# Optimization experiments

Measured on AMD Instinct MI355X. Metric: run time of the kernel, lower is better.

The kernel has to match this reference:

```python
import jax, jax.numpy as jnp
import numpy as np

N = 20000
E = 100000
EB = 20000
WIDTH = 32
KER_W = 64
KER_IN = 6
DEPTH = 4


def setup_inputs() -> dict:
    key = jax.random.key(0)
    ks = jax.random.split(key, 24)
    d = {}
    d["x"] = jax.random.normal(ks[0], (N, 1), dtype=jnp.float32)
    d["edge_index"] = jax.random.randint(ks[1], (2, E), 0, N)
    d["edge_attr"] = jax.random.uniform(ks[2], (E, KER_IN), dtype=jnp.float32)
    d["edge_index_boundary"] = jax.random.randint(ks[3], (2, EB), 0, N)
    d["edge_attr_boundary"] = jax.random.uniform(ks[4], (EB, KER_IN), dtype=jnp.float32)
    s = 0.1
    d["fc1_w"] = jax.random.normal(ks[5], (1, WIDTH), dtype=jnp.float32) * s
    d["fc1_b"] = jnp.zeros((WIDTH,), jnp.float32)
    d["fc2_w"] = jax.random.normal(ks[6], (WIDTH, 1), dtype=jnp.float32) * s
    d["fc2_b"] = jnp.zeros((1,), jnp.float32)
    for i, pfx in enumerate(["k1", "k2"]):
        o = 7 + i * 5
        d[pfx + "_w1"] = jax.random.normal(ks[o], (KER_IN, KER_W), dtype=jnp.float32) * s
        d[pfx + "_b1"] = jnp.zeros((KER_W,), jnp.float32)
        d[pfx + "_w2"] = jax.random.normal(ks[o + 1], (KER_W, KER_W), dtype=jnp.float32) * s
        d[pfx + "_b2"] = jnp.zeros((KER_W,), jnp.float32)
        d[pfx + "_w3"] = jax.random.normal(ks[o + 2], (KER_W, WIDTH * WIDTH), dtype=jnp.float32) * s
        d[pfx + "_b3"] = jnp.zeros((WIDTH * WIDTH,), jnp.float32)
        d[("root1", "root2")[i]] = jax.random.normal(ks[o + 3], (WIDTH, WIDTH), dtype=jnp.float32) * s
        d[("bias1", "bias2")[i]] = jnp.zeros((WIDTH,), jnp.float32)
    return d


def _nnconv(h, ei, ea, w1, b1, w2, b2, w3, b3, root, bias):
    # kernel MLP on edge_attr -> per-edge [in, out] weight
    k = jax.nn.relu(ea @ w1 + b1)
    k = jax.nn.relu(k @ w2 + b2)
    w = (k @ w3 + b3).reshape(-1, WIDTH, WIDTH)  # [E, in, out]
    msg = jnp.einsum('ei,eio->eo', h[ei[0]], w)  # gather + per-edge matmul
    agg = jax.ops.segment_sum(msg, ei[1], num_segments=N)
    cnt = jax.ops.segment_sum(jnp.ones((ei.shape[1],), h.dtype), ei[1], num_segments=N)
    agg = agg / jnp.maximum(cnt, 1.0)[:, None]  # mean aggregation
    return agg + h @ root + bias


def reference(x, edge_index, edge_attr, edge_index_boundary, edge_attr_boundary,
              fc1_w, fc1_b, fc2_w, fc2_b,
              k1_w1, k1_b1, k1_w2, k1_b2, k1_w3, k1_b3, root1, bias1,
              k2_w1, k2_b1, k2_w2, k2_b2, k2_w3, k2_b3, root2, bias2):
    h0 = x @ fc1_w + fc1_b  # fc1(data.x), reused every depth step
    h = h0
    for _ in range(DEPTH):
        h = (_nnconv(h, edge_index, edge_attr, k1_w1, k1_b1, k1_w2, k1_b2, k1_w3, k1_b3, root1, bias1)
             + _nnconv(h, edge_index_boundary, edge_attr_boundary, k2_w1, k2_b1, k2_w2, k2_b2, k2_w3, k2_b3, root2, bias2))
        h = jax.nn.relu(h) + h0
    return h @ fc2_w + fc2_b
```

## Files before the change

kernel.cpp:

```cpp
#include <hip/hip_runtime.h>
#include <cstdint>
#include <cstddef>

#define NN    20000
#define EM    100000
#define EBN   20000
#define WID   32
#define KW    64
#define KIN   6
#define NDEPTH 4
#define GC    2080
#define NBL   6
#define GR    2084
#define NQ    520
#define TPB_F 576


__global__ void k_count4(const int* __restrict__ ei, const int* __restrict__ eib,
                         int* __restrict__ cs1, int* __restrict__ cnt1,
                         int* __restrict__ csb, int* __restrict__ cntb) {
    int t = blockIdx.x * blockDim.x + threadIdx.x;
    if (t < EM) atomicAdd(&cs1[ei[t]], 1);
    else if (t < 2 * EM) atomicAdd(&cnt1[ei[t]], 1);
    else if (t < 2 * EM + EBN) atomicAdd(&csb[eib[t - 2 * EM]], 1);
    else if (t < 2 * EM + 2 * EBN) atomicAdd(&cntb[eib[t - 2 * EM]], 1);
}

__global__ void k_inv2(const int* __restrict__ cnt1, float* __restrict__ inv1,
                       const int* __restrict__ cntb, float* __restrict__ invb) {
    int i = blockIdx.x * blockDim.x + threadIdx.x;
    if (i < NN) {
        int c = cnt1[i]; if (c < 1) c = 1;
        inv1[i] = 1.0f / (float)c;
    } else if (i < 2 * NN) {
        int c = cntb[i - NN]; if (c < 1) c = 1;
        invb[i - NN] = 1.0f / (float)c;
    }
}


__global__ __launch_bounds__(1024) void k_scan3(
        const int* __restrict__ csA, int* __restrict__ curA, int* __restrict__ arankA,
        int* __restrict__ anodesA, int* __restrict__ aoffA, int* __restrict__ dnaA, int EA,
        const int* __restrict__ csB, int* __restrict__ curB, int* __restrict__ arankB,
        int* __restrict__ anodesB, int* __restrict__ aoffB, int* __restrict__ dnaB, int EB) {
    __shared__ int part[1024];
    __shared__ int partf[1024];
    const int* cnt; int *cur, *arank, *anodes, *aoff, *dna; int E;
    if (blockIdx.x == 0) { cnt = csA; cur = curA; arank = arankA; anodes = anodesA; aoff = aoffA; dna = dnaA; E = EA; }
    else                 { cnt = csB; cur = curB; arank = arankB; anodes = anodesB; aoff = aoffB; dna = dnaB; E = EB; }
    int t = threadIdx.x;
    int per = (NN + 1023) / 1024;
    int base = t * per;
    int s = 0, f = 0;
    for (int i = 0; i < per; i++) {
        int idx = base + i;
        if (idx < NN) { int c = cnt[idx]; s += c; f += (c > 0) ? 1 : 0; }
    }
    part[t] = s; partf[t] = f;
    __syncthreads();
    for (int od = 1; od < 1024; od <<= 1) {
        int v  = (t >= od) ? part[t - od] : 0;
        int vf = (t >= od) ? partf[t - od] : 0;
        __syncthreads();
        part[t] += v; partf[t] += vf;
        __syncthreads();
    }
    int run  = (t > 0) ? part[t - 1] : 0;
    int runf = (t > 0) ? partf[t - 1] : 0;
    for (int i = 0; i < per; i++) {
        int idx = base + i;
        if (idx < NN) {
            int c = cnt[idx];
            cur[idx] = run;
            arank[idx] = runf;
            if (c > 0) { anodes[runf] = idx; aoff[runf] = run; runf++; }
            run += c;
        }
    }
    if (t == 1023) { dna[0] = partf[1023]; aoff[partf[1023]] = E; }
}


__global__ void k_scatter3(const int* __restrict__ ei, int* __restrict__ cur1,
                           int* __restrict__ perm1, const int* __restrict__ eib,
                           int* __restrict__ curb, int* __restrict__ permb) {
    int t = blockIdx.x * blockDim.x + threadIdx.x;
    if (t < EM) { int p = atomicAdd(&cur1[ei[t]], 1); perm1[p] = t; }
    else if (t < EM + EBN) {
        int e = t - EM;
        int p = atomicAdd(&curb[eib[e]], 1); permb[p] = e;
    }
}

__global__ void k_permidx3(const int* __restrict__ ei, const int* __restrict__ perm1,
                           const int* __restrict__ arank1, int* __restrict__ rk1,
                           int* __restrict__ dst1,
                           const int* __restrict__ eib, const int* __restrict__ permb,
                           const int* __restrict__ arankb, int* __restrict__ rkb,
                           int* __restrict__ dstb) {
    int t = blockIdx.x * blockDim.x + threadIdx.x;
    if (t < EM) {
        int e = perm1[t];
        rk1[t] = arank1[ei[e]];
        dst1[t] = ei[EM + e];
    } else if (t < EM + EBN) {
        int i = t - EM;
        int e = permb[i];
        rkb[i] = arankb[eib[e]];
        dstb[i] = eib[EBN + e];
    }
}


__global__ void k_permM3(const float* __restrict__ w3a, const float* __restrict__ b3a,
                         float* __restrict__ M1,
                         const float* __restrict__ w3b, const float* __restrict__ b3b,
                         float* __restrict__ M2,
                         const float* __restrict__ r1, const float* __restrict__ b1,
                         const float* __restrict__ r2, const float* __restrict__ b2,
                         float* __restrict__ rs, float* __restrict__ bs) {
    int t = blockIdx.x * blockDim.x + threadIdx.x;
    if (t < 32 * GC) {
        int i = t / GC, c = t % GC;
        M1[t] = (c < 2048) ? w3a[(c >> 5) * 1024 + i * 32 + (c & 31)]
                           : b3a[i * 32 + (c - 2048)];
    } else if (t < 64 * GC) {
        int u = t - 32 * GC;
        int i = u / GC, c = u % GC;
        M2[u] = (c < 2048) ? w3b[(c >> 5) * 1024 + i * 32 + (c & 31)]
                           : b3b[i * 32 + (c - 2048)];
    } else if (t < 64 * GC + 1024) {
        int i = t - 64 * GC;
        rs[i] = r1[i] + r2[i];
    } else if (t < 64 * GC + 1056) {
        int i = t - 64 * GC - 1024;
        bs[i] = b1[i] + b2[i];
    }
}


__global__ __launch_bounds__(256) void k_mlp3(
        const float* __restrict__ ea1, const int* __restrict__ perm1,
        const float* __restrict__ w1a, const float* __restrict__ b1a,
        const float* __restrict__ w2a, const float* __restrict__ b2a,
        float* __restrict__ K1,
        const float* __restrict__ ea2, const int* __restrict__ permb,
        const float* __restrict__ w1b, const float* __restrict__ b1b,
        const float* __restrict__ w2b, const float* __restrict__ b2b,
        float* __restrict__ K2, int nmb) {
    __shared__ float sw1[KIN * KW];
    __shared__ float sw2[KW * KW];
    __shared__ float sb1[KW];
    __shared__ float sb2[KW];
    const float *ea, *w1, *b1, *w2, *b2;
    const int* perm;
    float* K;
    int e, E;
    if ((int)blockIdx.x < nmb) {
        ea = ea1; perm = perm1; w1 = w1a; b1 = b1a; w2 = w2a; b2 = b2a; K = K1;
        e = blockIdx.x * 256 + threadIdx.x; E = EM;
    } else {
        ea = ea2; perm = permb; w1 = w1b; b1 = b1b; w2 = w2b; b2 = b2b; K = K2;
        e = (blockIdx.x - nmb) * 256 + threadIdx.x; E = EBN;
    }
    for (int i = threadIdx.x; i < KIN * KW; i += 256) sw1[i] = w1[i];
    for (int i = threadIdx.x; i < KW * KW; i += 256)  sw2[i] = w2[i];
    if (threadIdx.x < KW) { sb1[threadIdx.x] = b1[threadIdx.x]; sb2[threadIdx.x] = b2[threadIdx.x]; }
    __syncthreads();
    if (e >= E) return;
    int eo = perm[e];
    float a0 = ea[(size_t)eo * KIN + 0];
    float a1 = ea[(size_t)eo * KIN + 1];
    float a2 = ea[(size_t)eo * KIN + 2];
    float a3 = ea[(size_t)eo * KIN + 3];
    float a4 = ea[(size_t)eo * KIN + 4];
    float a5 = ea[(size_t)eo * KIN + 5];
    float t[KW];
#pragma unroll
    for (int j = 0; j < KW; j++) {
        float s = sb1[j];
        s += a0 * sw1[0 * KW + j];
        s += a1 * sw1[1 * KW + j];
        s += a2 * sw1[2 * KW + j];
        s += a3 * sw1[3 * KW + j];
        s += a4 * sw1[4 * KW + j];
        s += a5 * sw1[5 * KW + j];
        t[j] = fmaxf(s, 0.0f);
    }
#pragma unroll
    for (int h = 0; h < 2; h++) {
        int j0 = h * 32;
        float4 acc[8];
#pragma unroll
        for (int jj = 0; jj < 8; jj++)
            acc[jj] = *(const float4*)&sb2[j0 + jj * 4];
#pragma unroll
        for (int c = 0; c < KW; c++) {
            float tc = t[c];
#pragma unroll
            for (int jj = 0; jj < 8; jj++) {
                float4 w = *(const float4*)&sw2[c * KW + j0 + jj * 4];
                acc[jj].x += tc * w.x; acc[jj].y += tc * w.y;
                acc[jj].z += tc * w.z; acc[jj].w += tc * w.w;
            }
        }
#pragma unroll
        for (int jj = 0; jj < 8; jj++) {
            float4 r = acc[jj];
            r.x = fmaxf(r.x, 0.f); r.y = fmaxf(r.y, 0.f);
            r.z = fmaxf(r.z, 0.f); r.w = fmaxf(r.w, 0.f);
            *(float4*)&K[(size_t)e * KW + j0 + jj * 4] = r;
        }
    }
}


__global__ void k_h0g(const float* __restrict__ x, const float* __restrict__ fc1w,
        const float* __restrict__ fc1b, float* __restrict__ h,
        const int* __restrict__ arank1, const int* __restrict__ anodes1,
        const int* __restrict__ dna1, float* __restrict__ hg1,
        const int* __restrict__ arankb, const int* __restrict__ anodesb,
        const int* __restrict__ dnab, float* __restrict__ hgb) {
    int t = blockIdx.x * blockDim.x + threadIdx.x;
    if (t < NN * WID) {
        int n = t >> 5, j = t & 31;
        float v = x[n] * fc1w[j] + fc1b[j];
        h[t] = v;
        int r = arank1[n];
        if (r < dna1[0] && anodes1[r] == n)
            hg1[(r / NBL) * 256 + j * 8 + (r % NBL)] = v;
    } else if (t < 2 * NN * WID) {
        int u = t - NN * WID;
        int n = u >> 5, j = u & 31;
        int r = arankb[n];
        if (r < dnab[0] && anodesb[r] == n)
            hgb[(r / NBL) * 256 + j * 8 + (r % NBL)] = x[n] * fc1w[j] + fc1b[j];
    }
}


__global__ __launch_bounds__(TPB_F, 3) void k_fuse3(
        const int* __restrict__ rkA, const int* __restrict__ dstA,
        const int* __restrict__ aoffA, const int* __restrict__ dnaA,
        const float* __restrict__ KA, const float* __restrict__ MA,
        const float* __restrict__ hgA, float* __restrict__ aggA,
        const int* __restrict__ rkB, const int* __restrict__ dstB,
        const int* __restrict__ aoffB, const int* __restrict__ dnaB,
        const float* __restrict__ KB, const float* __restrict__ MB,
        const float* __restrict__ hgB, float* __restrict__ aggB,
        int nblkA) {
    __shared__ float sG[NBL * GR];
    const int *rk_s, *dst_s, *aoff;
    const float *Ks, *M, *hg;
    float* agg;
    int bid, na;
    if ((int)blockIdx.x < nblkA) {
        bid = blockIdx.x; na = dnaA[0];
        rk_s = rkA; dst_s = dstA; aoff = aoffA; Ks = KA; M = MA; hg = hgA; agg = aggA;
    } else {
        bid = blockIdx.x - nblkA; na = dnaB[0];
        rk_s = rkB; dst_s = dstB; aoff = aoffB; Ks = KB; M = MB; hg = hgB; agg = aggB;
    }
    int a0 = bid * NBL;
    if (a0 >= na) return;
    int t = threadIdx.x;
    if (t < NQ) {
        int col = t * 4;
        const float* hb = hg + (size_t)bid * 256;
        float4 acc[NBL];
#pragma unroll
        for (int r = 0; r < NBL; r++) acc[r] = make_float4(0.f, 0.f, 0.f, 0.f);
#pragma unroll 8
        for (int k = 0; k < 32; k++) {
            float4 mv = *(const float4*)&M[(size_t)k * GC + col];
            float4 ha = *(const float4*)&hb[k * 8];
            float2 hc = *(const float2*)&hb[k * 8 + 4];
            float hv[NBL] = {ha.x, ha.y, ha.z, ha.w, hc.x, hc.y};
#pragma unroll
            for (int r = 0; r < NBL; r++) {
                acc[r].x += hv[r] * mv.x; acc[r].y += hv[r] * mv.y;
                acc[r].z += hv[r] * mv.z; acc[r].w += hv[r] * mv.w;
            }
        }
#pragma unroll
        for (int r = 0; r < NBL; r++)
            *(float4*)&sG[r * GR + col] = acc[r];
    }
    __syncthreads();
    int a1 = a0 + NBL; if (a1 > na) a1 = na;
    int e_lo = aoff[a0];
    int e_hi = aoff[a1];
    int g = t >> 3;
    int q4 = (t & 7) * 4;
    for (int e = e_lo + g; e < e_hi; e += TPB_F / 8) {
        int row = rk_s[e] - a0;
        int dst = dst_s[e];
        const float* Kr = Ks + (size_t)e * KW;
        int gb = row * GR;
        float4 v0 = *(const float4*)&sG[gb + 2048 + q4];
        float4 v1 = make_float4(0.f, 0.f, 0.f, 0.f);
        float4 v2 = v1, v3 = v1;
#pragma unroll
        for (int c4 = 0; c4 < 16; c4++) {
            float4 kv = *(const float4*)&Kr[c4 * 4];
            float4 g0 = *(const float4*)&sG[gb + (c4 * 4 + 0) * 32 + q4];
            float4 g1 = *(const float4*)&sG[gb + (c4 * 4 + 1) * 32 + q4];
            float4 g2 = *(const float4*)&sG[gb + (c4 * 4 + 2) * 32 + q4];
            float4 g3 = *(const float4*)&sG[gb + (c4 * 4 + 3) * 32 + q4];
            v0.x += kv.x * g0.x; v0.y += kv.x * g0.y; v0.z += kv.x * g0.z; v0.w += kv.x * g0.w;
            v1.x += kv.y * g1.x; v1.y += kv.y * g1.y; v1.z += kv.y * g1.z; v1.w += kv.y * g1.w;
            v2.x += kv.z * g2.x; v2.y += kv.z * g2.y; v2.z += kv.z * g2.z; v2.w += kv.z * g2.w;
            v3.x += kv.w * g3.x; v3.y += kv.w * g3.y; v3.z += kv.w * g3.z; v3.w += kv.w * g3.w;
        }
        float4 m;
        m.x = v0.x + v1.x + v2.x + v3.x;
        m.y = v0.y + v1.y + v2.y + v3.y;
        m.z = v0.z + v1.z + v2.z + v3.z;
        m.w = v0.w + v1.w + v2.w + v3.w;
        float* ap = agg + (size_t)dst * WID + q4;
        unsafeAtomicAdd(ap + 0, m.x);
        unsafeAtomicAdd(ap + 1, m.y);
        unsafeAtomicAdd(ap + 2, m.z);
        unsafeAtomicAdd(ap + 3, m.w);
    }
}


__global__ __launch_bounds__(256) void k_node2(float* __restrict__ h,
        const float* __restrict__ agg1, const float* __restrict__ aggb,
        const float* __restrict__ inv1, const float* __restrict__ invb,
        const float* __restrict__ x, const float* __restrict__ fc1w,
        const float* __restrict__ fc1b,
        const float* __restrict__ rs, const float* __restrict__ bs,
        const int* __restrict__ arank1, const int* __restrict__ anodes1,
        const int* __restrict__ dna1, float* __restrict__ hg1,
        const int* __restrict__ arankb, const int* __restrict__ anodesb,
        const int* __restrict__ dnab, float* __restrict__ hgb) {
    __shared__ float sR[1024];
    __shared__ float sB[32];
    for (int i = threadIdx.x; i < 1024; i += 256) sR[i] = rs[i];
    if (threadIdx.x < 32) sB[threadIdx.x] = bs[threadIdx.x];
    __syncthreads();
    int t = blockIdx.x * 256 + threadIdx.x;
    if (t >= NN * WID) return;
    int n = t >> 5, j = t & 31;
    float s = agg1[t] * inv1[n] + aggb[t] * invb[n] + sB[j];
    const float* hr = h + (size_t)n * WID;
#pragma unroll
    for (int i = 0; i < 32; i++) s += hr[i] * sR[i * 32 + j];
    float h0v = x[n] * fc1w[j] + fc1b[j];
    float val = fmaxf(s, 0.0f) + h0v;
    h[t] = val;
    int r1 = arank1[n];
    if (r1 < dna1[0] && anodes1[r1] == n)
        hg1[(r1 / NBL) * 256 + j * 8 + (r1 % NBL)] = val;
    int rb = arankb[n];
    if (rb < dnab[0] && anodesb[rb] == n)
        hgb[(rb / NBL) * 256 + j * 8 + (rb % NBL)] = val;
}

__global__ void k_fc2(const float* __restrict__ h, const float* __restrict__ w,
                      const float* __restrict__ b, float* __restrict__ out) {
    int n = blockIdx.x * blockDim.x + threadIdx.x;
    if (n >= NN) return;
    const float4* hv = (const float4*)(h + (size_t)n * WID);
    const float4* wv = (const float4*)w;
    float s = b[0];
#pragma unroll
    for (int q = 0; q < 8; q++) {
        float4 a = hv[q], c = wv[q];
        s += a.x * c.x + a.y * c.y + a.z * c.z + a.w * c.w;
    }
    out[n] = s;
}


extern "C" void kernel_launch(void* const* d_in, const int* in_sizes, int n_in,
                              void* d_out, int out_size, void* d_ws, size_t ws_size,
                              hipStream_t stream) {
    const float* x    = (const float*)d_in[0];
    const int*   ei   = (const int*)d_in[1];
    const float* ea   = (const float*)d_in[2];
    const int*   eib  = (const int*)d_in[3];
    const float* eab  = (const float*)d_in[4];
    const float* fc1w = (const float*)d_in[5];
    const float* fc1b = (const float*)d_in[6];
    const float* fc2w = (const float*)d_in[7];
    const float* fc2b = (const float*)d_in[8];
    const float* k1w1 = (const float*)d_in[9];
    const float* k1b1 = (const float*)d_in[10];
    const float* k1w2 = (const float*)d_in[11];
    const float* k1b2 = (const float*)d_in[12];
    const float* k1w3 = (const float*)d_in[13];
    const float* k1b3 = (const float*)d_in[14];
    const float* root1= (const float*)d_in[15];
    const float* bias1= (const float*)d_in[16];
    const float* k2w1 = (const float*)d_in[17];
    const float* k2b1 = (const float*)d_in[18];
    const float* k2w2 = (const float*)d_in[19];
    const float* k2b2 = (const float*)d_in[20];
    const float* k2w3 = (const float*)d_in[21];
    const float* k2b3 = (const float*)d_in[22];
    const float* root2= (const float*)d_in[23];
    const float* bias2= (const float*)d_in[24];

    float* p = (float*)d_ws;
    auto alloc = [&](size_t nflt) { float* r = p; p += nflt; return r; };
    float* K1   = alloc((size_t)EM * KW);
    float* Kb   = alloc((size_t)EBN * KW);
    float* hA   = alloc((size_t)NN * WID);
    float* agg1 = alloc((size_t)NN * WID);
    float* aggb = alloc((size_t)NN * WID);
    float* hg1  = alloc((size_t)3400 * 256);
    float* hgb  = alloc((size_t)3400 * 256);
    float* inv1 = alloc(NN);
    float* invb = alloc(NN);
    float* rs   = alloc(1024);
    float* bs   = alloc(32);
    int*   cnt1 = (int*)alloc(NN);
    int*   cntb = (int*)alloc(NN);
    int*   cs1  = (int*)alloc(NN);
    int*   csb  = (int*)alloc(NN);
    int*   cur1 = (int*)alloc(NN);
    int*   curb = (int*)alloc(NN);
    int*   arank1 = (int*)alloc(NN);
    int*   arankb = (int*)alloc(NN);
    int*   anodes1= (int*)alloc(NN);
    int*   anodesb= (int*)alloc(NN);
    int*   aoff1  = (int*)alloc(NN + 1);
    int*   aoffb  = (int*)alloc(NN + 1);
    int*   dna1   = (int*)alloc(1);
    int*   dnab   = (int*)alloc(1);
    int*   perm1= (int*)alloc(EM);
    int*   permb= (int*)alloc(EBN);
    int*   rk1  = (int*)alloc(EM);
    int*   dst1 = (int*)alloc(EM);
    int*   rkb  = (int*)alloc(EBN);
    int*   dstb = (int*)alloc(EBN);
    float* M1   = alloc(32 * GC);
    float* M2   = alloc(32 * GC);

    hipMemsetAsync(cnt1, 0, 4 * NN * sizeof(int), stream);
    k_count4<<<(2 * EM + 2 * EBN + 255) / 256, 256, 0, stream>>>(ei, eib, cs1, cnt1, csb, cntb);
    k_scan3<<<2, 1024, 0, stream>>>(cs1, cur1, arank1, anodes1, aoff1, dna1, EM,
                                    csb, curb, arankb, anodesb, aoffb, dnab, EBN);
    k_inv2<<<(2 * NN + 255) / 256, 256, 0, stream>>>(cnt1, inv1, cntb, invb);
    k_scatter3<<<(EM + EBN + 255) / 256, 256, 0, stream>>>(ei, cur1, perm1, eib, curb, permb);
    k_permidx3<<<(EM + EBN + 255) / 256, 256, 0, stream>>>(ei, perm1, arank1, rk1, dst1,
                                                           eib, permb, arankb, rkb, dstb);
    int nmb = (EM + 255) / 256;
    k_mlp3<<<nmb + (EBN + 255) / 256, 256, 0, stream>>>(
        ea, perm1, k1w1, k1b1, k1w2, k1b2, K1,
        eab, permb, k2w1, k2b1, k2w2, k2b2, Kb, nmb);
    k_permM3<<<(64 * GC + 1056 + 255) / 256, 256, 0, stream>>>(
        k1w3, k1b3, M1, k2w3, k2b3, M2, root1, bias1, root2, bias2, rs, bs);
    k_h0g<<<(2 * NN * WID + 255) / 256, 256, 0, stream>>>(x, fc1w, fc1b, hA,
                                                          arank1, anodes1, dna1, hg1,
                                                          arankb, anodesb, dnab, hgb);

    int nblkA = (NN + NBL - 1) / NBL;
    int fgrid = nblkA * 2;
    for (int d = 0; d < NDEPTH; d++) {
        hipMemsetAsync(agg1, 0, (size_t)2 * NN * WID * sizeof(float), stream);
        k_fuse3<<<fgrid, TPB_F, 0, stream>>>(rk1, dst1, aoff1, dna1, K1, M1, hg1, agg1,
                                             rkb, dstb, aoffb, dnab, Kb, M2, hgb, aggb,
                                             nblkA);
        k_node2<<<(NN * WID + 255) / 256, 256, 0, stream>>>(hA, agg1, aggb, inv1, invb,
                                                            x, fc1w, fc1b, rs, bs,
                                                            arank1, anodes1, dna1, hg1,
                                                            arankb, anodesb, dnab, hgb);
    }
    k_fc2<<<(NN + 255) / 256, 256, 0, stream>>>(hA, fc2w, fc2b, (float*)d_out);
}
```

Measured before the change: 595.3 us.

## Split fused edge kernel by kernel-MLP hidden halves with 12-node source blocks

Each block now handles 12 source nodes instead of 6. The 64 hidden channels of the per-node G=h·M precompute are split into two halves that go to separate blocks, so each block stages half as much G per node in shared memory and reads only 32 of the K entries per edge. The hg staging layout changes to 16 slots per feature to match. The aim is better reuse of M and of the edge loop, at the cost of twice the atomic adds into agg, since both halves add partial messages.

```diff
diff --git a/kernel.cpp b/kernel.cpp
--- a/kernel.cpp
+++ b/kernel.cpp
@@ -10,10 +10,11 @@
 #define KIN   6
 #define NDEPTH 4
 #define GC    2080
-#define NBL   6
-#define GR    2084
-#define NQ    520
+#define NBL   12
+#define CGR   1060
+#define NQH   264
 #define TPB_F 576
+#define NBH   1667
 
 
 __global__ void k_count4(const int* __restrict__ ei, const int* __restrict__ eib,
@@ -216,6 +217,8 @@
 }
 
 
+__device__ __forceinline__ int hslot(int rr) { return rr + ((rr >= 6) ? 2 : 0); }
+
 __global__ void k_h0g(const float* __restrict__ x, const float* __restrict__ fc1w,
         const float* __restrict__ fc1b, float* __restrict__ h,
         const int* __restrict__ arank1, const int* __restrict__ anodes1,
@@ -229,18 +232,18 @@
         h[t] = v;
         int r = arank1[n];
         if (r < dna1[0] && anodes1[r] == n)
-            hg1[(r / NBL) * 256 + j * 8 + (r % NBL)] = v;
+            hg1[(r / NBL) * 512 + j * 16 + hslot(r % NBL)] = v;
     } else if (t < 2 * NN * WID) {
         int u = t - NN * WID;
         int n = u >> 5, j = u & 31;
         int r = arankb[n];
         if (r < dnab[0] && anodesb[r] == n)
-            hgb[(r / NBL) * 256 + j * 8 + (r % NBL)] = x[n] * fc1w[j] + fc1b[j];
-    }
-}
-
-
-__global__ __launch_bounds__(TPB_F, 3) void k_fuse3(
+            hgb[(r / NBL) * 512 + j * 16 + hslot(r % NBL)] = x[n] * fc1w[j] + fc1b[j];
+    }
+}
+
+
+__global__ __launch_bounds__(TPB_F, 3) void k_fuse5(
         const int* __restrict__ rkA, const int* __restrict__ dstA,
         const int* __restrict__ aoffA, const int* __restrict__ dnaA,
         const float* __restrict__ KA, const float* __restrict__ MA,
@@ -248,44 +251,52 @@
         const int* __restrict__ rkB, const int* __restrict__ dstB,
         const int* __restrict__ aoffB, const int* __restrict__ dnaB,
         const float* __restrict__ KB, const float* __restrict__ MB,
-        const float* __restrict__ hgB, float* __restrict__ aggB,
-        int nblkA) {
-    __shared__ float sG[NBL * GR];
+        const float* __restrict__ hgB, float* __restrict__ aggB) {
+    __shared__ float sG[NBL * CGR];
     const int *rk_s, *dst_s, *aoff;
     const float *Ks, *M, *hg;
     float* agg;
-    int bid, na;
-    if ((int)blockIdx.x < nblkA) {
-        bid = blockIdx.x; na = dnaA[0];
+    int b = blockIdx.x;
+    int na;
+    if (b < 2 * NBH) {
+        na = dnaA[0];
         rk_s = rkA; dst_s = dstA; aoff = aoffA; Ks = KA; M = MA; hg = hgA; agg = aggA;
     } else {
-        bid = blockIdx.x - nblkA; na = dnaB[0];
+        b -= 2 * NBH; na = dnaB[0];
         rk_s = rkB; dst_s = dstB; aoff = aoffB; Ks = KB; M = MB; hg = hgB; agg = aggB;
     }
+    int half = (b >= NBH) ? 1 : 0;
+    int bid = b - half * NBH;
     int a0 = bid * NBL;
     if (a0 >= na) return;
     int t = threadIdx.x;
-    if (t < NQ) {
-        int col = t * 4;
-        const float* hb = hg + (size_t)bid * 256;
-        float4 acc[NBL];
-#pragma unroll
-        for (int r = 0; r < NBL; r++) acc[r] = make_float4(0.f, 0.f, 0.f, 0.f);
+    int nq = half ? NQH : 256;
+    if (t < 2 * NQH) {
+        int rg = (t >= NQH) ? 1 : 0;
+        int q = t - rg * NQH;
+        if (q < nq) {
+            int cc = q * 4;
+            const float* hb = hg + (size_t)bid * 512 + rg * 8;
+            const float* Mcol = M + half * 1024 + cc;
+            float4 acc[6];
+#pragma unroll
+            for (int r = 0; r < 6; r++) acc[r] = make_float4(0.f, 0.f, 0.f, 0.f);
 #pragma unroll 8
-        for (int k = 0; k < 32; k++) {
-            float4 mv = *(const float4*)&M[(size_t)k * GC + col];
-            float4 ha = *(const float4*)&hb[k * 8];
-            float2 hc = *(const float2*)&hb[k * 8 + 4];
-            float hv[NBL] = {ha.x, ha.y, ha.z, ha.w, hc.x, hc.y};
-#pragma unroll
-            for (int r = 0; r < NBL; r++) {
-                acc[r].x += hv[r] * mv.x; acc[r].y += hv[r] * mv.y;
-                acc[r].z += hv[r] * mv.z; acc[r].w += hv[r] * mv.w;
+            for (int k = 0; k < 32; k++) {
+                float4 mv = *(const float4*)&Mcol[(size_t)k * GC];
+                float4 ha = *(const float4*)&hb[k * 16];
+                float2 hc = *(const float2*)&hb[k * 16 + 4];
+                float hv[6] = {ha.x, ha.y, ha.z, ha.w, hc.x, hc.y};
+#pragma unroll
+                for (int r = 0; r < 6; r++) {
+                    acc[r].x += hv[r] * mv.x; acc[r].y += hv[r] * mv.y;
+                    acc[r].z += hv[r] * mv.z; acc[r].w += hv[r] * mv.w;
+                }
             }
+#pragma unroll
+            for (int r = 0; r < 6; r++)
+                *(float4*)&sG[(rg * 6 + r) * CGR + cc] = acc[r];
         }
-#pragma unroll
-        for (int r = 0; r < NBL; r++)
-            *(float4*)&sG[r * GR + col] = acc[r];
     }
     __syncthreads();
     int a1 = a0 + NBL; if (a1 > na) a1 = na;
@@ -296,13 +307,15 @@
     for (int e = e_lo + g; e < e_hi; e += TPB_F / 8) {
         int row = rk_s[e] - a0;
         int dst = dst_s[e];
-        const float* Kr = Ks + (size_t)e * KW;
-        int gb = row * GR;
-        float4 v0 = *(const float4*)&sG[gb + 2048 + q4];
+        const float* Kr = Ks + (size_t)e * KW + half * 32;
+        int gb = row * CGR;
+        float4 v0;
+        if (half) v0 = *(const float4*)&sG[gb + 1024 + q4];
+        else      v0 = make_float4(0.f, 0.f, 0.f, 0.f);
         float4 v1 = make_float4(0.f, 0.f, 0.f, 0.f);
         float4 v2 = v1, v3 = v1;
 #pragma unroll
-        for (int c4 = 0; c4 < 16; c4++) {
+        for (int c4 = 0; c4 < 8; c4++) {
             float4 kv = *(const float4*)&Kr[c4 * 4];
             float4 g0 = *(const float4*)&sG[gb + (c4 * 4 + 0) * 32 + q4];
             float4 g1 = *(const float4*)&sG[gb + (c4 * 4 + 1) * 32 + q4];
@@ -354,10 +367,10 @@
     h[t] = val;
     int r1 = arank1[n];
     if (r1 < dna1[0] && anodes1[r1] == n)
-        hg1[(r1 / NBL) * 256 + j * 8 + (r1 % NBL)] = val;
+        hg1[(r1 / NBL) * 512 + j * 16 + hslot(r1 % NBL)] = val;
     int rb = arankb[n];
     if (rb < dnab[0] && anodesb[rb] == n)
-        hgb[(rb / NBL) * 256 + j * 8 + (rb % NBL)] = val;
+        hgb[(rb / NBL) * 512 + j * 16 + hslot(rb % NBL)] = val;
 }
 
 __global__ void k_fc2(const float* __restrict__ h, const float* __restrict__ w,
@@ -412,8 +425,8 @@
     float* hA   = alloc((size_t)NN * WID);
     float* agg1 = alloc((size_t)NN * WID);
     float* aggb = alloc((size_t)NN * WID);
-    float* hg1  = alloc((size_t)3400 * 256);
-    float* hgb  = alloc((size_t)3400 * 256);
+    float* hg1  = alloc((size_t)(NBH + 2) * 512);
+    float* hgb  = alloc((size_t)(NBH + 2) * 512);
     float* inv1 = alloc(NN);
     float* invb = alloc(NN);
     float* rs   = alloc(1024);
@@ -459,13 +472,11 @@
                                                           arank1, anodes1, dna1, hg1,
                                                           arankb, anodesb, dnab, hgb);
 
-    int nblkA = (NN + NBL - 1) / NBL;
-    int fgrid = nblkA * 2;
+    int fgrid = 4 * NBH;
     for (int d = 0; d < NDEPTH; d++) {
         hipMemsetAsync(agg1, 0, (size_t)2 * NN * WID * sizeof(float), stream);
-        k_fuse3<<<fgrid, TPB_F, 0, stream>>>(rk1, dst1, aoff1, dna1, K1, M1, hg1, agg1,
-                                             rkb, dstb, aoffb, dnab, Kb, M2, hgb, aggb,
-                                             nblkA);
+        k_fuse5<<<fgrid, TPB_F, 0, stream>>>(rk1, dst1, aoff1, dna1, K1, M1, hg1, agg1,
+                                             rkb, dstb, aoffb, dnab, Kb, M2, hgb, aggb);
         k_node2<<<(NN * WID + 255) / 256, 256, 0, stream>>>(hA, agg1, aggb, inv1, invb,
                                                             x, fc1w, fc1b, rs, bs,
                                                             arank1, anodes1, dna1, hg1,
```

Result: slower. 948.1 us (+59.3%).
